# Performance work log

Measured on AMD Instinct MI355X. Metric: run time of the kernel, lower is better.

## Reference

```python
import jax, jax.numpy as jnp
import numpy as np

N_NODES = 100000
N_EDGES = 1600000
N_GRAPHS = 64
D_IN = 64
D_HID = 64
D_OUT = 64


def gcn_conv(x, W, b, src, dst, n):
    """PyG-style GCNConv: x' = D^-1/2 (A+I) D^-1/2 (x W) + b."""
    xw = x @ W  # [N, d_out]
    loops = jnp.arange(n, dtype=src.dtype)
    s = jnp.concatenate([src, loops])  # add self-loops
    d = jnp.concatenate([dst, loops])
    deg = jax.ops.segment_sum(jnp.ones_like(d, dtype=xw.dtype), d, num_segments=n)
    dinv = jax.lax.rsqrt(jnp.maximum(deg, 1.0))
    coef = dinv[s] * dinv[d]  # [E+N]
    msg = xw[s] * coef[:, None]  # gather + scale, [E+N, d_out]
    out = jax.ops.segment_sum(msg, d, num_segments=n)  # scatter-add
    return out + b


def global_mean_pool(h, batch, num_graphs):
    sums = jax.ops.segment_sum(h, batch, num_segments=num_graphs)
    cnt = jax.ops.segment_sum(jnp.ones((h.shape[0],), h.dtype), batch, num_segments=num_graphs)
    return sums / jnp.maximum(cnt, 1.0)[:, None]


def setup_inputs() -> dict:
    key = jax.random.key(0)
    ks = jax.random.split(key, 8)
    x = jax.random.normal(ks[0], (N_NODES, D_IN), dtype=jnp.float32)
    edge_index = jax.random.randint(ks[1], (2, N_EDGES), 0, N_NODES, dtype=jnp.int64 if jax.config.jax_enable_x64 else jnp.int32)
    batch = jnp.sort(jax.random.randint(ks[2], (N_NODES,), 0, N_GRAPHS))
    sc = lambda fan_in: 1.0 / np.sqrt(fan_in)
    W1 = jax.random.uniform(ks[3], (D_IN, D_HID), jnp.float32, -sc(D_IN), sc(D_IN))
    b1 = jnp.zeros((D_HID,), jnp.float32)
    W2 = jax.random.uniform(ks[4], (D_HID, D_HID), jnp.float32, -sc(D_HID), sc(D_HID))
    b2 = jnp.zeros((D_HID,), jnp.float32)
    Wp = jax.random.uniform(ks[5], (D_HID, D_OUT), jnp.float32, -sc(D_HID), sc(D_HID))
    bp = jax.random.uniform(ks[6], (D_OUT,), jnp.float32, -sc(D_HID), sc(D_HID))
    return {"x": x, "edge_index": edge_index, "batch": batch,
            "W1": W1, "b1": b1, "W2": W2, "b2": b2, "Wp": Wp, "bp": bp}


def reference(x, edge_index, batch, W1, b1, W2, b2, Wp, bp):
    src, dst = edge_index[0], edge_index[1]
    n = x.shape[0]
    h = jax.nn.relu(gcn_conv(x, W1, b1, src, dst, n))
    h = jax.nn.relu(gcn_conv(h, W2, b2, src, dst, n))
    hg = global_mean_pool(h, batch, N_GRAPHS)  # [G, d_hid]
    return hg @ Wp + bp  # [G, d_out]
```

## Files before the change

### kernel.cpp

```cpp
#include <hip/hip_runtime.h>
#include <hip/hip_fp16.h>


#define DF 64
#define BSH 7
#define BNODES 128
#define CAP 4096

struct alignas(8) h4 { __half2 a, b; };


__global__ __launch_bounds__(256) void part_kernel(
        const int* __restrict__ src, const int* __restrict__ dst,
        const int4* __restrict__ src4, const int4* __restrict__ dst4,
        int E, unsigned* __restrict__ bedges, int* __restrict__ bucketCur, int nb) {
    __shared__ int lcnt[1024];
    __shared__ int lbase[1024];
    int tid = threadIdx.x;
    for (int t = tid; t < nb; t += 256) lcnt[t] = 0;
    __syncthreads();
    int nq = E >> 2;
    unsigned packed[32];
    int bkt[32];
    int rk[32];
    int qbase = blockIdx.x * 2048;
#pragma unroll
    for (int c = 0; c < 8; c++) {
        int qi = qbase + c * 256 + tid;
        int4 s = {0, 0, 0, 0}, d = {0, 0, 0, 0};
        bool v = qi < nq;
        if (v) { s = src4[qi]; d = dst4[qi]; }
        packed[4*c+0] = (unsigned)s.x | ((unsigned)(d.x & (BNODES-1)) << 24);
        packed[4*c+1] = (unsigned)s.y | ((unsigned)(d.y & (BNODES-1)) << 24);
        packed[4*c+2] = (unsigned)s.z | ((unsigned)(d.z & (BNODES-1)) << 24);
        packed[4*c+3] = (unsigned)s.w | ((unsigned)(d.w & (BNODES-1)) << 24);
        bkt[4*c+0] = v ? (d.x >> BSH) : -1;
        bkt[4*c+1] = v ? (d.y >> BSH) : -1;
        bkt[4*c+2] = v ? (d.z >> BSH) : -1;
        bkt[4*c+3] = v ? (d.w >> BSH) : -1;
    }
#pragma unroll
    for (int j = 0; j < 32; j++)
        rk[j] = (bkt[j] >= 0) ? atomicAdd(&lcnt[bkt[j]], 1) : 0;
    __syncthreads();
    for (int t = tid; t < nb; t += 256)
        lbase[t] = lcnt[t] ? atomicAdd(&bucketCur[t], lcnt[t]) : 0;
    __syncthreads();
#pragma unroll
    for (int j = 0; j < 32; j++) {
        if (bkt[j] >= 0) {
            int pos = lbase[bkt[j]] + rk[j];
            if (pos < CAP) bedges[(size_t)bkt[j] * CAP + pos] = packed[j];
        }
    }
    if (blockIdx.x == 0 && tid < (E & 3)) {
        int e = nq * 4 + tid;
        int sv = src[e], dv = dst[e];
        int b = dv >> BSH;
        int pos = atomicAdd(&bucketCur[b], 1);
        if (pos < CAP)
            bedges[(size_t)b * CAP + pos] =
                (unsigned)sv | ((unsigned)(dv & (BNODES-1)) << 24);
    }
}

__global__ void part_scalar_kernel(const int* __restrict__ src, const int* __restrict__ dst,
                                   int E, unsigned* __restrict__ bedges,
                                   int* __restrict__ bucketCur) {
    int stride = gridDim.x * blockDim.x;
    for (int e = blockIdx.x * blockDim.x + threadIdx.x; e < E; e += stride) {
        int sv = src[e], dv = dst[e];
        int b = dv >> BSH;
        int pos = atomicAdd(&bucketCur[b], 1);
        if (pos < CAP)
            bedges[(size_t)b * CAP + pos] =
                (unsigned)sv | ((unsigned)(dv & (BNODES-1)) << 24);
    }
}


__global__ __launch_bounds__(256) void sort_kernel(
        unsigned* __restrict__ bedges, const int* __restrict__ bucketCur,
        int* __restrict__ offs, float* __restrict__ dinv, int N) {
    __shared__ unsigned ein[CAP];
    __shared__ unsigned eout[CAP];
    __shared__ int cnt[BNODES];
    __shared__ int sc[BNODES];
    __shared__ int off[BNODES + 1];
    __shared__ int cur[BNODES];
    int b = blockIdx.x, tid = threadIdx.x;
    int n = min(bucketCur[b], CAP);
    unsigned* gp = bedges + (size_t)b * CAP;
    if (tid < BNODES) cnt[tid] = 0;
    __syncthreads();
    for (int i = tid; i < n; i += 256) {
        unsigned u = gp[i];
        ein[i] = u;
        atomicAdd(&cnt[u >> 24], 1);
    }
    __syncthreads();
    if (tid < BNODES) sc[tid] = cnt[tid];
    __syncthreads();
    for (int d = 1; d < BNODES; d <<= 1) {
        int v = (tid >= d && tid < BNODES) ? sc[tid - d] : 0;
        __syncthreads();
        if (tid < BNODES) sc[tid] += v;
        __syncthreads();
    }
    if (tid < BNODES) {
        off[tid + 1] = sc[tid];
        cur[tid] = sc[tid] - cnt[tid];
        if (tid == 0) off[0] = 0;
    }
    __syncthreads();
    for (int i = tid; i < n; i += 256) {
        unsigned u = ein[i];
        int p = atomicAdd(&cur[u >> 24], 1);
        eout[p] = u;
    }
    __syncthreads();
    for (int i = tid; i < n; i += 256) gp[i] = eout[i];
    if (tid <= BNODES) offs[(size_t)b * (BNODES + 1) + tid] = off[tid];
    int node = (b << BSH) + tid;
    if (tid < BNODES && node < N)
        dinv[node] = 1.0f / sqrtf((float)(cnt[tid] + 1));
}


__global__ void gemm_scale(const float4* __restrict__ X4, const float4* __restrict__ W4,
                           const float* __restrict__ dinv, h4* __restrict__ Y2, int n) {
    __shared__ float4 Wl4[64][16];
    __shared__ float Xl[16][68];
    int tid = threadIdx.x;
    float4* Wf = &Wl4[0][0];
#pragma unroll
    for (int i = 0; i < 4; i++) {
        int idx = tid + i * 256;
        Wf[idx] = W4[idx];
    }
    int row0 = blockIdx.x * 16;
    int r = tid >> 4, c4 = tid & 15;
    {
        int row = row0 + r;
        float4 v = (row < n) ? X4[(size_t)row * 16 + c4] : float4{0.f, 0.f, 0.f, 0.f};
        Xl[r][c4 * 4 + 0] = v.x;
        Xl[r][c4 * 4 + 1] = v.y;
        Xl[r][c4 * 4 + 2] = v.z;
        Xl[r][c4 * 4 + 3] = v.w;
    }
    __syncthreads();
    float ax = 0.f, ay = 0.f, az = 0.f, aw = 0.f;
#pragma unroll
    for (int k = 0; k < 64; k++) {
        float xv = Xl[r][k];
        float4 w = Wl4[k][c4];
        ax += xv * w.x;
        ay += xv * w.y;
        az += xv * w.z;
        aw += xv * w.w;
    }
    int row = row0 + r;
    if (row < n) {
        float dv = dinv[row];
        h4 o;
        o.a = __floats2half2_rn(ax * dv, ay * dv);
        o.b = __floats2half2_rn(az * dv, aw * dv);
        Y2[(size_t)row * 16 + c4] = o;
    }
}

__global__ __launch_bounds__(256) void agg_kernel(
        const h4* __restrict__ Y2, const unsigned* __restrict__ bedges,
        const int* __restrict__ offs, const float* __restrict__ dinv,
        const float4* __restrict__ bias4, float4* __restrict__ H4, int N) {
    __shared__ unsigned eb[CAP];
    __shared__ int off[65];
    int blk = blockIdx.x;
    int b = blk >> 1, half = blk & 1;
    int tid = threadIdx.x;
    if (tid < 65) off[tid] = offs[(size_t)b * (BNODES + 1) + half * 64 + tid];
    __syncthreads();
    int e0 = off[0];
    int ecnt = off[64] - e0;
    const unsigned* gp = bedges + (size_t)b * CAP + e0;
    for (int i = tid; i < ecnt; i += 256) eb[i] = gp[i];
    __syncthreads();
    int gg = tid >> 4, q = tid & 15;
    float4 bq = bias4[q];
    for (int r = gg; r < 64; r += 16) {
        int s = off[r] - e0, e = off[r + 1] - e0;
        float4 A0 = {0.f, 0.f, 0.f, 0.f}, A1 = A0, A2 = A0, A3 = A0;
        int i = s;
        for (; i + 3 < e; i += 4) {
            unsigned u0 = eb[i], u1 = eb[i + 1], u2 = eb[i + 2], u3 = eb[i + 3];
            h4 w0 = Y2[(size_t)(u0 & 0xFFFFFFu) * 16 + q];
            h4 w1 = Y2[(size_t)(u1 & 0xFFFFFFu) * 16 + q];
            h4 w2 = Y2[(size_t)(u2 & 0xFFFFFFu) * 16 + q];
            h4 w3 = Y2[(size_t)(u3 & 0xFFFFFFu) * 16 + q];
            float2 p0a = __half22float2(w0.a), p0b = __half22float2(w0.b);
            float2 p1a = __half22float2(w1.a), p1b = __half22float2(w1.b);
            float2 p2a = __half22float2(w2.a), p2b = __half22float2(w2.b);
            float2 p3a = __half22float2(w3.a), p3b = __half22float2(w3.b);
            A0.x += p0a.x; A0.y += p0a.y; A0.z += p0b.x; A0.w += p0b.y;
            A1.x += p1a.x; A1.y += p1a.y; A1.z += p1b.x; A1.w += p1b.y;
            A2.x += p2a.x; A2.y += p2a.y; A2.z += p2b.x; A2.w += p2b.y;
            A3.x += p3a.x; A3.y += p3a.y; A3.z += p3b.x; A3.w += p3b.y;
        }
        for (; i < e; i++) {
            unsigned u = eb[i];
            h4 w = Y2[(size_t)(u & 0xFFFFFFu) * 16 + q];
            float2 pa = __half22float2(w.a), pb = __half22float2(w.b);
            A0.x += pa.x; A0.y += pa.y; A0.z += pb.x; A0.w += pb.y;
        }
        int node = (b << BSH) + half * 64 + r;
        if (node < N) {
            float4 S;
            S.x = A0.x + A1.x + A2.x + A3.x;
            S.y = A0.y + A1.y + A2.y + A3.y;
            S.z = A0.z + A1.z + A2.z + A3.z;
            S.w = A0.w + A1.w + A2.w + A3.w;
            h4 sv = Y2[(size_t)node * 16 + q];
            float2 s1 = __half22float2(sv.a), s2 = __half22float2(sv.b);
            float dv = dinv[node];
            float4 o;
            o.x = fmaxf(dv * (S.x + s1.x) + bq.x, 0.f);
            o.y = fmaxf(dv * (S.y + s1.y) + bq.y, 0.f);
            o.z = fmaxf(dv * (S.z + s2.x) + bq.z, 0.f);
            o.w = fmaxf(dv * (S.w + s2.y) + bq.w, 0.f);
            H4[(size_t)node * 16 + q] = o;
        }
    }
}


__global__ void pool_kernel(const float4* __restrict__ H4, const int* __restrict__ batch,
                            float* __restrict__ sums, int* __restrict__ cnts, int n) {
    int gw = (blockIdx.x * blockDim.x + threadIdx.x) >> 6;
    int lane = threadIdx.x & 63;
    int g = lane >> 4, q = lane & 15;
    int start = gw * 256;
    if (start >= n) return;
    int end = min(start + 256, n);
    float ax = 0.f, ay = 0.f, az = 0.f, aw = 0.f;
    int cur = -1, run = 0;
    for (int i = start + g; i < end; i += 4) {
        int b = batch[i];
        if (b != cur) {
            if (run > 0) {
                atomicAdd(&sums[cur * DF + q * 4 + 0], ax);
                atomicAdd(&sums[cur * DF + q * 4 + 1], ay);
                atomicAdd(&sums[cur * DF + q * 4 + 2], az);
                atomicAdd(&sums[cur * DF + q * 4 + 3], aw);
                if (q == 0) atomicAdd(&cnts[cur], run);
            }
            cur = b; run = 0;
            ax = ay = az = aw = 0.f;
        }
        float4 v = H4[(size_t)i * 16 + q];
        ax += v.x; ay += v.y; az += v.z; aw += v.w;
        run++;
    }
    if (run > 0) {
        atomicAdd(&sums[cur * DF + q * 4 + 0], ax);
        atomicAdd(&sums[cur * DF + q * 4 + 1], ay);
        atomicAdd(&sums[cur * DF + q * 4 + 2], az);
        atomicAdd(&sums[cur * DF + q * 4 + 3], aw);
        if (q == 0) atomicAdd(&cnts[cur], run);
    }
}

__global__ void final_kernel(const float* __restrict__ sums, const int* __restrict__ cnts,
                             const float* __restrict__ Wp, const float* __restrict__ bp,
                             float* __restrict__ out) {
    int g = blockIdx.x, j = threadIdx.x;
    __shared__ float hg[64];
    float c = fmaxf((float)cnts[g], 1.f);
    hg[j] = sums[g * DF + j] / c;
    __syncthreads();
    float acc = bp[j];
#pragma unroll
    for (int k = 0; k < 64; k++) acc += hg[k] * Wp[k * DF + j];
    out[g * DF + j] = acc;
}


extern "C" void kernel_launch(void* const* d_in, const int* in_sizes, int n_in,
                              void* d_out, int out_size, void* d_ws, size_t ws_size,
                              hipStream_t stream) {
    const float* x     = (const float*)d_in[0];
    const int*   ei    = (const int*)d_in[1];
    const int*   batch = (const int*)d_in[2];
    const float* W1    = (const float*)d_in[3];
    const float* b1    = (const float*)d_in[4];
    const float* W2    = (const float*)d_in[5];
    const float* b2    = (const float*)d_in[6];
    const float* Wp    = (const float*)d_in[7];
    const float* bp    = (const float*)d_in[8];

    int N = in_sizes[0] / DF;
    int E = in_sizes[1] / 2;
    const int* src = ei;
    const int* dst = ei + E;
    int NB = (N + BNODES - 1) >> BSH;
    int quadOK = ((E & 3) == 0) && (((uintptr_t)ei & 15) == 0) && (((uintptr_t)dst & 15) == 0);

    char* ws = (char*)d_ws;
    auto alloc = [&](size_t bytes) {
        void* p = (void*)ws;
        ws += (bytes + 255) / 256 * 256;
        return p;
    };
    float*    dinv      = (float*)alloc((size_t)N * 4);
    int*      bucketCur = (int*)alloc((size_t)NB * 4);
    unsigned* bedges    = (unsigned*)alloc((size_t)NB * CAP * 4);
    int*      offs      = (int*)alloc((size_t)NB * (BNODES + 1) * 4);
    h4*       y2        = (h4*)alloc((size_t)N * DF * 2);
    float*    h         = (float*)alloc((size_t)N * DF * 4);
    float*    psums     = (float*)alloc(64 * DF * 4);
    int*      pcnt      = (int*)alloc(64 * 4);

    hipMemsetAsync(bucketCur, 0, (size_t)NB * 4, stream);
    hipMemsetAsync(psums, 0, 64 * DF * 4 + 256, stream);

    if (quadOK) {
        int nq = E >> 2;
        int pblocks = (nq + 2047) / 2048;
        part_kernel<<<pblocks, 256, 0, stream>>>(src, dst, (const int4*)src, (const int4*)dst,
                                                 E, bedges, bucketCur, NB);
    } else {
        part_scalar_kernel<<<1024, 256, 0, stream>>>(src, dst, E, bedges, bucketCur);
    }
    sort_kernel<<<NB, 256, 0, stream>>>(bedges, bucketCur, offs, dinv, N);

    gemm_scale<<<(N + 15) / 16, 256, 0, stream>>>((const float4*)x, (const float4*)W1, dinv,
                                                  y2, N);
    agg_kernel<<<2 * NB, 256, 0, stream>>>(y2, bedges, offs, dinv,
                                           (const float4*)b1, (float4*)h, N);
    gemm_scale<<<(N + 15) / 16, 256, 0, stream>>>((const float4*)h, (const float4*)W2, dinv,
                                                  y2, N);
    agg_kernel<<<2 * NB, 256, 0, stream>>>(y2, bedges, offs, dinv,
                                           (const float4*)b2, (float4*)h, N);

    int waves = (N + 255) / 256;
    pool_kernel<<<(waves + 3) / 4, 256, 0, stream>>>((const float4*)h, batch, psums, pcnt, N);
    final_kernel<<<64, 64, 0, stream>>>(psums, pcnt, Wp, bp, (float*)d_out);
}
```

Baseline: 251.4 us.

## Store hidden activations in fp16 and widen aggregation gathers to 16 bytes

The hidden activation buffer h is now written by the aggregation kernel in fp16 instead of fp32. The second GEMM and the pool kernel read fp16 through a new gemm_f16in variant and a converted pool loop. The aggregation kernel now uses 8 lanes per node, each gathering 16-byte h8 chunks, instead of 16 lanes with 8-byte loads, so each thread handles two rows. The two memsets are merged into one by placing the zeroed buffers contiguously. This cuts memory traffic for h and the number of gather transactions, at the cost of an extra rounding of activations to fp16 and fewer threads per node in the gather.

```diff
diff --git a/kernel.cpp b/kernel.cpp
--- a/kernel.cpp
+++ b/kernel.cpp
@@ -7,7 +7,8 @@
 #define BNODES 128
 #define CAP 4096
 
-struct alignas(8) h4 { __half2 a, b; };
+struct alignas(8)  h4 { __half2 a, b; };
+struct alignas(16) h8 { __half2 a, b, c, d; };
 
 
 __global__ __launch_bounds__(256) void part_kernel(
@@ -127,7 +128,7 @@
 }
 
 
-__global__ void gemm_scale(const float4* __restrict__ X4, const float4* __restrict__ W4,
+__global__ void gemm_f32in(const float4* __restrict__ X4, const float4* __restrict__ W4,
                            const float* __restrict__ dinv, h4* __restrict__ Y2, int n) {
     __shared__ float4 Wl4[64][16];
     __shared__ float Xl[16][68];
@@ -169,10 +170,63 @@
     }
 }
 
+__global__ void gemm_f16in(const h4* __restrict__ X2, const float4* __restrict__ W4,
+                           const float* __restrict__ dinv, h4* __restrict__ Y2, int n) {
+    __shared__ float4 Wl4[64][16];
+    __shared__ float Xl[16][68];
+    int tid = threadIdx.x;
+    float4* Wf = &Wl4[0][0];
+#pragma unroll
+    for (int i = 0; i < 4; i++) {
+        int idx = tid + i * 256;
+        Wf[idx] = W4[idx];
+    }
+    int row0 = blockIdx.x * 16;
+    int r = tid >> 4, c4 = tid & 15;
+    {
+        int row = row0 + r;
+        h4 hv = (row < n) ? X2[(size_t)row * 16 + c4] : h4{__half2{0, 0}, __half2{0, 0}};
+        float2 va = __half22float2(hv.a), vb = __half22float2(hv.b);
+        Xl[r][c4 * 4 + 0] = va.x;
+        Xl[r][c4 * 4 + 1] = va.y;
+        Xl[r][c4 * 4 + 2] = vb.x;
+        Xl[r][c4 * 4 + 3] = vb.y;
+    }
+    __syncthreads();
+    float ax = 0.f, ay = 0.f, az = 0.f, aw = 0.f;
+#pragma unroll
+    for (int k = 0; k < 64; k++) {
+        float xv = Xl[r][k];
+        float4 w = Wl4[k][c4];
+        ax += xv * w.x;
+        ay += xv * w.y;
+        az += xv * w.z;
+        aw += xv * w.w;
+    }
+    int row = row0 + r;
+    if (row < n) {
+        float dv = dinv[row];
+        h4 o;
+        o.a = __floats2half2_rn(ax * dv, ay * dv);
+        o.b = __floats2half2_rn(az * dv, aw * dv);
+        Y2[(size_t)row * 16 + c4] = o;
+    }
+}
+
+#define ACC8(A, w)                                        \
+    { float2 _p = __half22float2((w).a);                  \
+      A[0] += _p.x; A[1] += _p.y;                         \
+      _p = __half22float2((w).b);                         \
+      A[2] += _p.x; A[3] += _p.y;                         \
+      _p = __half22float2((w).c);                         \
+      A[4] += _p.x; A[5] += _p.y;                         \
+      _p = __half22float2((w).d);                         \
+      A[6] += _p.x; A[7] += _p.y; }
+
 __global__ __launch_bounds__(256) void agg_kernel(
-        const h4* __restrict__ Y2, const unsigned* __restrict__ bedges,
+        const h8* __restrict__ Y8, const unsigned* __restrict__ bedges,
         const int* __restrict__ offs, const float* __restrict__ dinv,
-        const float4* __restrict__ bias4, float4* __restrict__ H4, int N) {
+        const float* __restrict__ bias, h8* __restrict__ H8, int N) {
     __shared__ unsigned eb[CAP];
     __shared__ int off[65];
     int blk = blockIdx.x;
@@ -185,55 +239,53 @@
     const unsigned* gp = bedges + (size_t)b * CAP + e0;
     for (int i = tid; i < ecnt; i += 256) eb[i] = gp[i];
     __syncthreads();
-    int gg = tid >> 4, q = tid & 15;
-    float4 bq = bias4[q];
-    for (int r = gg; r < 64; r += 16) {
+    int gg = tid >> 3, q = tid & 7;
+    float bq[8];
+#pragma unroll
+    for (int j = 0; j < 8; j++) bq[j] = bias[q * 8 + j];
+#pragma unroll
+    for (int rr = 0; rr < 2; rr++) {
+        int r = gg + rr * 32;
         int s = off[r] - e0, e = off[r + 1] - e0;
-        float4 A0 = {0.f, 0.f, 0.f, 0.f}, A1 = A0, A2 = A0, A3 = A0;
+        float A0[8], A1[8], A2[8], A3[8];
+#pragma unroll
+        for (int j = 0; j < 8; j++) { A0[j] = 0.f; A1[j] = 0.f; A2[j] = 0.f; A3[j] = 0.f; }
         int i = s;
         for (; i + 3 < e; i += 4) {
             unsigned u0 = eb[i], u1 = eb[i + 1], u2 = eb[i + 2], u3 = eb[i + 3];
-            h4 w0 = Y2[(size_t)(u0 & 0xFFFFFFu) * 16 + q];
-            h4 w1 = Y2[(size_t)(u1 & 0xFFFFFFu) * 16 + q];
-            h4 w2 = Y2[(size_t)(u2 & 0xFFFFFFu) * 16 + q];
-            h4 w3 = Y2[(size_t)(u3 & 0xFFFFFFu) * 16 + q];
-            float2 p0a = __half22float2(w0.a), p0b = __half22float2(w0.b);
-            float2 p1a = __half22float2(w1.a), p1b = __half22float2(w1.b);
-            float2 p2a = __half22float2(w2.a), p2b = __half22float2(w2.b);
-            float2 p3a = __half22float2(w3.a), p3b = __half22float2(w3.b);
-            A0.x += p0a.x; A0.y += p0a.y; A0.z += p0b.x; A0.w += p0b.y;
-            A1.x += p1a.x; A1.y += p1a.y; A1.z += p1b.x; A1.w += p1b.y;
-            A2.x += p2a.x; A2.y += p2a.y; A2.z += p2b.x; A2.w += p2b.y;
-            A3.x += p3a.x; A3.y += p3a.y; A3.z += p3b.x; A3.w += p3b.y;
+            h8 w0 = Y8[(size_t)(u0 & 0xFFFFFFu) * 8 + q];
+            h8 w1 = Y8[(size_t)(u1 & 0xFFFFFFu) * 8 + q];
+            h8 w2 = Y8[(size_t)(u2 & 0xFFFFFFu) * 8 + q];
+            h8 w3 = Y8[(size_t)(u3 & 0xFFFFFFu) * 8 + q];
+            ACC8(A0, w0); ACC8(A1, w1); ACC8(A2, w2); ACC8(A3, w3);
         }
         for (; i < e; i++) {
             unsigned u = eb[i];
-            h4 w = Y2[(size_t)(u & 0xFFFFFFu) * 16 + q];
-            float2 pa = __half22float2(w.a), pb = __half22float2(w.b);
-            A0.x += pa.x; A0.y += pa.y; A0.z += pb.x; A0.w += pb.y;
+            h8 w = Y8[(size_t)(u & 0xFFFFFFu) * 8 + q];
+            ACC8(A0, w);
         }
         int node = (b << BSH) + half * 64 + r;
         if (node < N) {
-            float4 S;
-            S.x = A0.x + A1.x + A2.x + A3.x;
-            S.y = A0.y + A1.y + A2.y + A3.y;
-            S.z = A0.z + A1.z + A2.z + A3.z;
-            S.w = A0.w + A1.w + A2.w + A3.w;
-            h4 sv = Y2[(size_t)node * 16 + q];
-            float2 s1 = __half22float2(sv.a), s2 = __half22float2(sv.b);
+            h8 sv = Y8[(size_t)node * 8 + q];
+            float S[8];
+            ACC8(A0, sv);
+#pragma unroll
+            for (int j = 0; j < 8; j++) S[j] = A0[j] + A1[j] + A2[j] + A3[j];
             float dv = dinv[node];
-            float4 o;
-            o.x = fmaxf(dv * (S.x + s1.x) + bq.x, 0.f);
-            o.y = fmaxf(dv * (S.y + s1.y) + bq.y, 0.f);
-            o.z = fmaxf(dv * (S.z + s2.x) + bq.z, 0.f);
-            o.w = fmaxf(dv * (S.w + s2.y) + bq.w, 0.f);
-            H4[(size_t)node * 16 + q] = o;
+#pragma unroll
+            for (int j = 0; j < 8; j++) S[j] = fmaxf(dv * S[j] + bq[j], 0.f);
+            h8 o;
+            o.a = __floats2half2_rn(S[0], S[1]);
+            o.b = __floats2half2_rn(S[2], S[3]);
+            o.c = __floats2half2_rn(S[4], S[5]);
+            o.d = __floats2half2_rn(S[6], S[7]);
+            H8[(size_t)node * 8 + q] = o;
         }
     }
 }
 
 
-__global__ void pool_kernel(const float4* __restrict__ H4, const int* __restrict__ batch,
+__global__ void pool_kernel(const h4* __restrict__ H2, const int* __restrict__ batch,
                             float* __restrict__ sums, int* __restrict__ cnts, int n) {
     int gw = (blockIdx.x * blockDim.x + threadIdx.x) >> 6;
     int lane = threadIdx.x & 63;
@@ -256,8 +308,9 @@
             cur = b; run = 0;
             ax = ay = az = aw = 0.f;
         }
-        float4 v = H4[(size_t)i * 16 + q];
-        ax += v.x; ay += v.y; az += v.z; aw += v.w;
+        h4 hv = H2[(size_t)i * 16 + q];
+        float2 va = __half22float2(hv.a), vb = __half22float2(hv.b);
+        ax += va.x; ay += va.y; az += vb.x; aw += vb.y;
         run++;
     }
     if (run > 0) {
@@ -310,17 +363,22 @@
         ws += (bytes + 255) / 256 * 256;
         return p;
     };
+    size_t zBucketCur = 0;
+    size_t zPsums     = ((size_t)NB * 4 + 255) / 256 * 256;
+    size_t zPcnt      = zPsums + 64 * DF * 4;
+    size_t zTotal     = zPcnt + 256;
+    char*     zbase     = (char*)alloc(zTotal);
+    int*      bucketCur = (int*)(zbase + zBucketCur);
+    float*    psums     = (float*)(zbase + zPsums);
+    int*      pcnt      = (int*)(zbase + zPcnt);
+
     float*    dinv      = (float*)alloc((size_t)N * 4);
-    int*      bucketCur = (int*)alloc((size_t)NB * 4);
     unsigned* bedges    = (unsigned*)alloc((size_t)NB * CAP * 4);
     int*      offs      = (int*)alloc((size_t)NB * (BNODES + 1) * 4);
     h4*       y2        = (h4*)alloc((size_t)N * DF * 2);
-    float*    h         = (float*)alloc((size_t)N * DF * 4);
-    float*    psums     = (float*)alloc(64 * DF * 4);
-    int*      pcnt      = (int*)alloc(64 * 4);
-
-    hipMemsetAsync(bucketCur, 0, (size_t)NB * 4, stream);
-    hipMemsetAsync(psums, 0, 64 * DF * 4 + 256, stream);
+    h4*       h2        = (h4*)alloc((size_t)N * DF * 2);
+
+    hipMemsetAsync(zbase, 0, zTotal, stream);
 
     if (quadOK) {
         int nq = E >> 2;
@@ -332,16 +390,16 @@
     }
     sort_kernel<<<NB, 256, 0, stream>>>(bedges, bucketCur, offs, dinv, N);
 
-    gemm_scale<<<(N + 15) / 16, 256, 0, stream>>>((const float4*)x, (const float4*)W1, dinv,
+    gemm_f32in<<<(N + 15) / 16, 256, 0, stream>>>((const float4*)x, (const float4*)W1, dinv,
                                                   y2, N);
-    agg_kernel<<<2 * NB, 256, 0, stream>>>(y2, bedges, offs, dinv,
-                                           (const float4*)b1, (float4*)h, N);
-    gemm_scale<<<(N + 15) / 16, 256, 0, stream>>>((const float4*)h, (const float4*)W2, dinv,
+    agg_kernel<<<2 * NB, 256, 0, stream>>>((const h8*)y2, bedges, offs, dinv,
+                                           b1, (h8*)h2, N);
+    gemm_f16in<<<(N + 15) / 16, 256, 0, stream>>>(h2, (const float4*)W2, dinv,
                                                   y2, N);
-    agg_kernel<<<2 * NB, 256, 0, stream>>>(y2, bedges, offs, dinv,
-                                           (const float4*)b2, (float4*)h, N);
+    agg_kernel<<<2 * NB, 256, 0, stream>>>((const h8*)y2, bedges, offs, dinv,
+                                           b2, (h8*)h2, N);
 
     int waves = (N + 255) / 256;
-    pool_kernel<<<(waves + 3) / 4, 256, 0, stream>>>((const float4*)h, batch, psums, pcnt, N);
+    pool_kernel<<<(waves + 3) / 4, 256, 0, stream>>>(h2, batch, psums, pcnt, N);
     final_kernel<<<64, 64, 0, stream>>>(psums, pcnt, Wp, bp, (float*)d_out);
 }
```

Result: faster. 242.7 us (-3.5%).
